# Kernel optimization log

Hardware: AMD Instinct MI355X
Metric: run time of the kernel (lower is better)

The kernel has to match this reference:

```python
import jax, jax.numpy as jnp
import numpy as np

N = 21  # nodes per graph (20 laser sectors + 1 robot node)
MAX_RANGE = 10.0
_bound = np.linspace(-np.pi / 2 - 0.03, np.pi / 2, 21, dtype=np.float32)[:-1]
_angles = _bound + np.float32(np.pi / 20)
ANGLE_FEAT = jnp.asarray(np.stack([np.sin(_angles), np.cos(_angles)], 1), dtype=jnp.float32)  # [20,2]


def _build_nodes(state24):
    # state24: [B,24] -> node features [B,21,7]
    B = state24.shape[0]
    laser = state24[:, :20, None] / MAX_RANGE                       # [B,20,1]
    angle = jnp.broadcast_to(ANGLE_FEAT[None], (B, 20, 2))          # [B,20,2]
    sector = jnp.concatenate([laser, angle, jnp.zeros((B, 20, 4), state24.dtype)], -1)  # [B,20,7]
    robot = jnp.concatenate([jnp.zeros((B, 1, 3), state24.dtype), state24[:, None, 20:]], -1)  # [B,1,7]
    return jnp.concatenate([sector, robot], axis=1)                 # [B,21,7]


def _gatv2(x, Wl, Wr, att, bias, heads, dim):
    # GATv2 over a fully-connected graph with self-loops (dense all-pairs).
    # e_ij = att . leaky_relu(Wl x_j + Wr x_i); alpha = softmax_j; out_i = sum_j alpha_ij (Wl x_j)
    B = x.shape[0]
    gl = (x @ Wl).reshape(B, N, heads, dim)  # source transform [B,j,H,D]
    gr = (x @ Wr).reshape(B, N, heads, dim)  # target transform [B,i,H,D]
    s = jax.nn.leaky_relu(gl[:, None] + gr[:, :, None], negative_slope=0.2)  # [B,i,j,H,D]
    e = jnp.einsum('bijhd,hd->bijh', s, att)                                  # [B,i,j,H]
    alpha = jax.nn.softmax(e, axis=2)                                          # softmax over sources j
    out = jnp.einsum('bijh,bjhd->bihd', alpha, gl).reshape(B, N, heads * dim)
    return out + bias


def setup_inputs() -> dict:
    key = jax.random.key(0)
    ks = jax.random.split(key, 16)
    r = lambda k, shape, s: (jax.random.normal(k, shape, dtype=jnp.float32) * s)
    B = 1024
    return {
        'state24': jax.random.normal(ks[0], (B, 24), dtype=jnp.float32),
        'Wl1': r(ks[1], (7, 256), 0.3), 'Wr1': r(ks[2], (7, 256), 0.3),
        'att1': r(ks[3], (4, 64), 0.1), 'b1': r(ks[4], (256,), 0.02),
        'Wl2': r(ks[5], (256, 64), 0.06), 'Wr2': r(ks[6], (256, 64), 0.06),
        'att2': r(ks[7], (1, 64), 0.1), 'b2': r(ks[8], (64,), 0.02),
        'fc1_w': r(ks[9], (64, 256), 0.12), 'fc1_b': r(ks[10], (256,), 0.02),
        'fc2_w': r(ks[11], (256, 256), 0.06), 'fc2_b': r(ks[12], (256,), 0.02),
        'fc3_w': r(ks[13], (256, 2), 0.06), 'fc3_b': r(ks[14], (2,), 0.02),
    }


def reference(state24, Wl1, Wr1, att1, b1, Wl2, Wr2, att2, b2,
              fc1_w, fc1_b, fc2_w, fc2_b, fc3_w, fc3_b):
    x = _build_nodes(state24)                               # [B,21,7]
    h = jax.nn.elu(_gatv2(x, Wl1, Wr1, att1, b1, 4, 64))    # [B,21,256]
    h = _gatv2(h, Wl2, Wr2, att2, b2, 1, 64)                # [B,21,64]
    nfv = jnp.mean(h, axis=1)                               # global_mean_pool -> [B,64]
    h = jax.nn.relu(nfv @ fc1_w + fc1_b)
    h = jax.nn.relu(h @ fc2_w + fc2_b)
    return jnp.tanh(h @ fc3_w + fc3_b)                      # [B,2]
```

## Files before the change

kernel.cpp:

```cpp
#include <hip/hip_runtime.h>
#include <hip/hip_fp16.h>
#include <math.h>

#define PI_D 3.141592653589793

typedef _Float16 h2 __attribute__((ext_vector_type(2)));
typedef _Float16 h4 __attribute__((ext_vector_type(4)));
typedef unsigned short us4 __attribute__((ext_vector_type(4)));
typedef __fp16 f16v2 __attribute__((ext_vector_type(2)));

#define STR1 260
#define STR1H 130
#define STR1Q 65
#define STR2 66

static __device__ __forceinline__ h2 pack_h2(float a, float b) {
    return __builtin_bit_cast(h2, __builtin_amdgcn_cvt_pkrtz(a, b));
}

static __device__ __forceinline__ float fdot2(h2 a, h2 b, float c) {
    return __builtin_amdgcn_fdot2(__builtin_bit_cast(f16v2, a),
                                  __builtin_bit_cast(f16v2, b), c, false);
}

static __device__ __forceinline__ h4 habs4(h4 x) {
    us4 u = __builtin_bit_cast(us4, x);
    us4 m = {0x7fff, 0x7fff, 0x7fff, 0x7fff};
    return __builtin_bit_cast(h4, (us4)(u & m));
}

__global__ __launch_bounds__(256, 4) void actor_fused_kernel(
    const float* __restrict__ state24,
    const float* __restrict__ Wl1, const float* __restrict__ Wr1,
    const float* __restrict__ att1, const float* __restrict__ b1,
    const float* __restrict__ Wl2, const float* __restrict__ Wr2,
    const float* __restrict__ att2, const float* __restrict__ b2,
    const float* __restrict__ fc1_w, const float* __restrict__ fc1_b,
    const float* __restrict__ fc2_w, const float* __restrict__ fc2_b,
    const float* __restrict__ fc3_w, const float* __restrict__ fc3_b,
    float* __restrict__ out, int B)
{
    const int bix = blockIdx.x;
    if (bix >= B) return;
    const int tid = threadIdx.x;

    __shared__ float sinL[20], cosL[20], laserL[20], robotL[4];
    __shared__ __align__(16) h2 attLh[128];
    __shared__ __align__(16) float att2L[64];
    __shared__ __align__(16) _Float16 gr1h[24 * STR1];
    __shared__ __align__(16) union {
        struct { _Float16 gl1h[21 * STR1]; float eP[1764]; } p1;
        struct { float gl2[24 * STR2]; float gr2[24 * STR2]; float e2[24 * 21];
                 float part[4][64]; float nfv[64]; float ha[256]; float hb[256]; } p2;
    } U;

    if (tid < 20) {
        double step = (PI_D + 0.03) / 20.0;
        float bound = (float)(-PI_D / 2.0 - 0.03 + (double)tid * step);
        float ang = bound + (float)(PI_D / 20.0);
        sinL[tid] = sinf(ang);
        cosL[tid] = cosf(ang);
        laserL[tid] = state24[bix * 24 + tid] * 0.1f;
    }
    if (tid >= 32 && tid < 36) robotL[tid - 32] = state24[bix * 24 + 20 + (tid - 32)];
    if (tid < 128) {
        float2 ap = ((const float2*)att1)[tid];
        attLh[tid] = pack_h2(ap.x, ap.y);
    }
    if (tid < 64) att2L[tid] = att2[tid];
    __syncthreads();

    {
        float wl[7], wr[7];
        #pragma unroll
        for (int k = 0; k < 7; k++) { wl[k] = Wl1[k * 256 + tid]; wr[k] = Wr1[k * 256 + tid]; }
        #pragma unroll
        for (int n = 0; n < 20; n++) {
            float l = laserL[n], s = sinL[n], c = cosL[n];
            U.p1.gl1h[n * STR1 + tid] = (_Float16)(l * wl[0] + s * wl[1] + c * wl[2]);
            gr1h[n * STR1 + tid]     = (_Float16)(l * wr[0] + s * wr[1] + c * wr[2]);
        }
        float r0 = robotL[0], r1 = robotL[1], r2 = robotL[2], r3 = robotL[3];
        U.p1.gl1h[20 * STR1 + tid] = (_Float16)(r0 * wl[3] + r1 * wl[4] + r2 * wl[5] + r3 * wl[6]);
        gr1h[20 * STR1 + tid]     = (_Float16)(r0 * wr[3] + r1 * wr[4] + r2 * wr[5] + r3 * wr[6]);
    }
    __syncthreads();

    {
        const int h = tid >> 6;
        const int lane = tid & 63;
        h4 areg[16];
        const h4* attH4 = (const h4*)attLh + h * 16;
        #pragma unroll
        for (int q = 0; q < 16; ++q) areg[q] = attH4[q];

        for (int it = 0; it < 7; ++it) {
            int q = it * 64 + lane;
            if (q < 441) {
                int i = q / 21;
                int j = q - i * 21;
                const h4* gA4 = (const h4*)(U.p1.gl1h + j * STR1 + h * 64);
                const h4* gB4 = (const h4*)(gr1h + i * STR1 + h * 64);
                float l0 = 0.f, l1 = 0.f, m0 = 0.f, m1 = 0.f;
                #pragma unroll
                for (int dp = 0; dp < 16; ++dp) {
                    h4 x = gA4[dp] + gB4[dp];
                    h4 ax = habs4(x);
                    h2 xl = __builtin_shufflevector(x, x, 0, 1);
                    h2 xh = __builtin_shufflevector(x, x, 2, 3);
                    h2 al = __builtin_shufflevector(areg[dp], areg[dp], 0, 1);
                    h2 ah = __builtin_shufflevector(areg[dp], areg[dp], 2, 3);
                    h2 axl = __builtin_shufflevector(ax, ax, 0, 1);
                    h2 axh = __builtin_shufflevector(ax, ax, 2, 3);
                    l0 = fdot2(xl, al, l0); m0 = fdot2(axl, al, m0);
                    l1 = fdot2(xh, ah, l1); m1 = fdot2(axh, ah, m1);
                }
                U.p1.eP[h * 441 + q] = 0.6f * (l0 + l1) + 0.4f * (m0 + m1);
            }
        }
    }
    __syncthreads();

    if (tid < 84) {
        float* row = U.p1.eP + tid * 21;
        float m = row[0];
        #pragma unroll
        for (int j = 1; j < 21; j++) m = fmaxf(m, row[j]);
        float s = 0.f;
        #pragma unroll
        for (int j = 0; j < 21; j++) { float v = __expf(row[j] - m); row[j] = v; s += v; }
        float r = 1.f / s;
        #pragma unroll
        for (int j = 0; j < 21; j++) row[j] *= r;
    }
    __syncthreads();

    {
        h2 zz = {(_Float16)0.f, (_Float16)0.f};
        for (int z = tid; z < 384; z += 256)
            ((h2*)gr1h)[(21 + (z >> 7)) * STR1H + (z & 127)] = zz;

        int p = tid & 127, gi = tid >> 7;
        int h = p >> 5;
        float2 bb = ((const float2*)b1)[p];
        const h2* gcol = (const h2*)U.p1.gl1h + p;
        for (int i = gi; i < 21; i += 2) {
            const float* al = U.p1.eP + (h * 21 + i) * 21;
            float a0 = 0.f, a1 = 0.f;
            #pragma unroll
            for (int j = 0; j < 21; ++j) {
                float alpha = al[j];
                h2 gv = gcol[j * STR1H];
                a0 = fmaf(alpha, (float)gv.x, a0);
                a1 = fmaf(alpha, (float)gv.y, a1);
            }
            float v0 = a0 + bb.x, v1 = a1 + bb.y;
            v0 = v0 > 0.f ? v0 : __expf(v0) - 1.f;
            v1 = v1 > 0.f ? v1 : __expf(v1) - 1.f;
            h2 o; o.x = (_Float16)v0; o.y = (_Float16)v1;
            ((h2*)gr1h)[i * STR1H + p] = o;
        }
    }
    __syncthreads();

    {
        int c = tid & 63, g = tid >> 6;
        float accL[6] = {0, 0, 0, 0, 0, 0}, accR[6] = {0, 0, 0, 0, 0, 0};
        const h4* hrow4 = (const h4*)gr1h;
        const float* pwl = Wl2 + c;
        const float* pwr = Wr2 + c;
        #pragma unroll 2
        for (int kk = 0; kk < 64; ++kk) {
            float wl0 = pwl[(4 * kk + 0) * 64], wl1 = pwl[(4 * kk + 1) * 64];
            float wl2_ = pwl[(4 * kk + 2) * 64], wl3 = pwl[(4 * kk + 3) * 64];
            float wr0 = pwr[(4 * kk + 0) * 64], wr1 = pwr[(4 * kk + 1) * 64];
            float wr2_ = pwr[(4 * kk + 2) * 64], wr3 = pwr[(4 * kk + 3) * 64];
            h2 wlA = pack_h2(wl0, wl1), wlB = pack_h2(wl2_, wl3);
            h2 wrA = pack_h2(wr0, wr1), wrB = pack_h2(wr2_, wr3);
            #pragma unroll
            for (int m = 0; m < 6; ++m) {
                int n = g + 4 * m;
                h4 hv = hrow4[n * STR1Q + kk];
                h2 lo = __builtin_shufflevector(hv, hv, 0, 1);
                h2 hi = __builtin_shufflevector(hv, hv, 2, 3);
                accL[m] = fdot2(lo, wlA, accL[m]);
                accL[m] = fdot2(hi, wlB, accL[m]);
                accR[m] = fdot2(lo, wrA, accR[m]);
                accR[m] = fdot2(hi, wrB, accR[m]);
            }
        }
        #pragma unroll
        for (int m = 0; m < 6; ++m) {
            int n = g + 4 * m;
            U.p2.gl2[n * STR2 + c] = accL[m];
            U.p2.gr2[n * STR2 + c] = accR[m];
        }
    }
    __syncthreads();

    for (int it = 0; it < 2; ++it) {
        int t = it * 256 + tid;
        if (t < 441) {
            int i = t / 21;
            int j = t - i * 21;
            const float2* gA = (const float2*)(U.p2.gl2 + j * STR2);
            const float2* gB = (const float2*)(U.p2.gr2 + i * STR2);
            const float2* aa = (const float2*)att2L;
            float l0 = 0.f, l1 = 0.f, m0 = 0.f, m1 = 0.f;
            #pragma unroll
            for (int dp = 0; dp < 32; ++dp) {
                float2 va = gA[dp], vb = gB[dp], a = aa[dp];
                float x0 = va.x + vb.x, x1 = va.y + vb.y;
                l0 = fmaf(a.x, x0, l0); m0 = fmaf(a.x, fabsf(x0), m0);
                l1 = fmaf(a.y, x1, l1); m1 = fmaf(a.y, fabsf(x1), m1);
            }
            U.p2.e2[t] = 0.6f * (l0 + l1) + 0.4f * (m0 + m1);
        }
    }
    __syncthreads();

    if (tid < 24) {
        float* row = U.p2.e2 + tid * 21;
        if (tid < 21) {
            float m = row[0];
            #pragma unroll
            for (int j = 1; j < 21; j++) m = fmaxf(m, row[j]);
            float s = 0.f;
            #pragma unroll
            for (int j = 0; j < 21; j++) { float v = __expf(row[j] - m); row[j] = v; s += v; }
            float r = 1.f / s;
            #pragma unroll
            for (int j = 0; j < 21; j++) row[j] *= r;
        } else {
            #pragma unroll
            for (int j = 0; j < 21; j++) row[j] = 0.f;
        }
    }
    __syncthreads();

    {
        int d = tid & 63, g = tid >> 6;
        float sacc = 0.f;
        #pragma unroll
        for (int m = 0; m < 6; ++m) {
            int i = g + 4 * m;
            const float* al = U.p2.e2 + i * 21;
            float acc = 0.f;
            #pragma unroll
            for (int j = 0; j < 21; ++j) acc = fmaf(al[j], U.p2.gl2[j * STR2 + d], acc);
            sacc += acc;
        }
        U.p2.part[g][d] = sacc;
    }
    __syncthreads();
    if (tid < 64) {
        U.p2.nfv[tid] = (U.p2.part[0][tid] + U.p2.part[1][tid] + U.p2.part[2][tid] + U.p2.part[3][tid])
                        * (1.f / 21.f) + b2[tid];
    }
    __syncthreads();

    {
        float acc = fc1_b[tid];
        #pragma unroll
        for (int k = 0; k < 64; k++) acc = fmaf(U.p2.nfv[k], fc1_w[k * 256 + tid], acc);
        U.p2.ha[tid] = fmaxf(acc, 0.f);
    }
    __syncthreads();

    {
        float acc = fc2_b[tid];
        #pragma unroll 8
        for (int k = 0; k < 256; k++) acc = fmaf(U.p2.ha[k], fc2_w[k * 256 + tid], acc);
        U.p2.hb[tid] = fmaxf(acc, 0.f);
    }
    __syncthreads();

    if (tid < 128) {
        int o = tid >> 6, l = tid & 63;
        float s = 0.f;
        #pragma unroll
        for (int m = 0; m < 4; m++) { int k = l + 64 * m; s = fmaf(U.p2.hb[k], fc3_w[k * 2 + o], s); }
        #pragma unroll
        for (int off = 32; off >= 1; off >>= 1) s += __shfl_down(s, off, 64);
        if (l == 0) out[bix * 2 + o] = tanhf(s + fc3_b[o]);
    }
}

extern "C" void kernel_launch(void* const* d_in, const int* in_sizes, int n_in,
                              void* d_out, int out_size, void* d_ws, size_t ws_size,
                              hipStream_t stream) {
    const float* state24 = (const float*)d_in[0];
    const float* Wl1 = (const float*)d_in[1];
    const float* Wr1 = (const float*)d_in[2];
    const float* att1 = (const float*)d_in[3];
    const float* b1 = (const float*)d_in[4];
    const float* Wl2 = (const float*)d_in[5];
    const float* Wr2 = (const float*)d_in[6];
    const float* att2 = (const float*)d_in[7];
    const float* b2 = (const float*)d_in[8];
    const float* fc1_w = (const float*)d_in[9];
    const float* fc1_b = (const float*)d_in[10];
    const float* fc2_w = (const float*)d_in[11];
    const float* fc2_b = (const float*)d_in[12];
    const float* fc3_w = (const float*)d_in[13];
    const float* fc3_b = (const float*)d_in[14];
    float* out = (float*)d_out;

    int B = in_sizes[0] / 24;
    actor_fused_kernel<<<B, 256, 0, stream>>>(
        state24, Wl1, Wr1, att1, b1, Wl2, Wr2, att2, b2,
        fc1_w, fc1_b, fc2_w, fc2_b, fc3_w, fc3_b, out, B);
}
```

Baseline: 136.6 us.

## Split linear leaky-ReLU term into per-node dots, widen LDS loads, split-K FC layers

New measurement: 134.2 us. No clear change (-1.8%).

```diff
diff --git a/kernel.cpp b/kernel.cpp
--- a/kernel.cpp
+++ b/kernel.cpp
@@ -6,12 +6,13 @@
 
 typedef _Float16 h2 __attribute__((ext_vector_type(2)));
 typedef _Float16 h4 __attribute__((ext_vector_type(4)));
-typedef unsigned short us4 __attribute__((ext_vector_type(4)));
+typedef _Float16 h8 __attribute__((ext_vector_type(8)));
+typedef unsigned short us8 __attribute__((ext_vector_type(8)));
 typedef __fp16 f16v2 __attribute__((ext_vector_type(2)));
 
-#define STR1 260
-#define STR1H 130
-#define STR1Q 65
+#define STR1 264
+#define STR1H 132
+#define STR1O 33
 #define STR2 66
 
 static __device__ __forceinline__ h2 pack_h2(float a, float b) {
@@ -23,10 +24,10 @@
                                   __builtin_bit_cast(f16v2, b), c, false);
 }
 
-static __device__ __forceinline__ h4 habs4(h4 x) {
-    us4 u = __builtin_bit_cast(us4, x);
-    us4 m = {0x7fff, 0x7fff, 0x7fff, 0x7fff};
-    return __builtin_bit_cast(h4, (us4)(u & m));
+static __device__ __forceinline__ h8 habs8(h8 x) {
+    us8 u = __builtin_bit_cast(us8, x);
+    us8 m = {0x7fff, 0x7fff, 0x7fff, 0x7fff, 0x7fff, 0x7fff, 0x7fff, 0x7fff};
+    return __builtin_bit_cast(h8, (us8)(u & m));
 }
 
 __global__ __launch_bounds__(256, 4) void actor_fused_kernel(
@@ -49,9 +50,9 @@
     __shared__ __align__(16) float att2L[64];
     __shared__ __align__(16) _Float16 gr1h[24 * STR1];
     __shared__ __align__(16) union {
-        struct { _Float16 gl1h[21 * STR1]; float eP[1764]; } p1;
-        struct { float gl2[24 * STR2]; float gr2[24 * STR2]; float e2[24 * 21];
-                 float part[4][64]; float nfv[64]; float ha[256]; float hb[256]; } p2;
+        struct { _Float16 gl1h[21 * STR1]; float eP[1764]; float uv[168]; } p1;
+        struct { float gl2[24 * STR2]; float gr2[24 * STR2]; float e2[504];
+                 float red[4][256]; float nfv[64]; float ha[256]; float hb[256]; } p2;
     } U;
 
     if (tid < 20) {
@@ -86,36 +87,52 @@
     }
     __syncthreads();
 
+    if (tid < 168) {
+        int r = tid < 84 ? tid : tid - 84;
+        int h = r / 21, idx = r - h * 21;
+        const _Float16* rowp = (tid < 84 ? U.p1.gl1h : gr1h) + idx * STR1 + h * 64;
+        const h8* row8 = (const h8*)rowp;
+        const h2* ar = attLh + h * 32;
+        float l0 = 0.f, l1 = 0.f;
+        #pragma unroll
+        for (int ch = 0; ch < 8; ++ch) {
+            h8 g = row8[ch];
+            l0 = fdot2(__builtin_shufflevector(g, g, 0, 1), ar[ch * 4 + 0], l0);
+            l1 = fdot2(__builtin_shufflevector(g, g, 2, 3), ar[ch * 4 + 1], l1);
+            l0 = fdot2(__builtin_shufflevector(g, g, 4, 5), ar[ch * 4 + 2], l0);
+            l1 = fdot2(__builtin_shufflevector(g, g, 6, 7), ar[ch * 4 + 3], l1);
+        }
+        U.p1.uv[tid] = l0 + l1;
+    }
+    __syncthreads();
+
     {
         const int h = tid >> 6;
         const int lane = tid & 63;
-        h4 areg[16];
-        const h4* attH4 = (const h4*)attLh + h * 16;
-        #pragma unroll
-        for (int q = 0; q < 16; ++q) areg[q] = attH4[q];
+        h2 ar[32];
+        #pragma unroll
+        for (int q = 0; q < 32; ++q) ar[q] = attLh[h * 32 + q];
+        const float* uvU = U.p1.uv + h * 21;
+        const float* uvV = U.p1.uv + 84 + h * 21;
 
         for (int it = 0; it < 7; ++it) {
             int q = it * 64 + lane;
             if (q < 441) {
                 int i = q / 21;
                 int j = q - i * 21;
-                const h4* gA4 = (const h4*)(U.p1.gl1h + j * STR1 + h * 64);
-                const h4* gB4 = (const h4*)(gr1h + i * STR1 + h * 64);
-                float l0 = 0.f, l1 = 0.f, m0 = 0.f, m1 = 0.f;
+                const h8* gA8 = (const h8*)(U.p1.gl1h + j * STR1 + h * 64);
+                const h8* gB8 = (const h8*)(gr1h + i * STR1 + h * 64);
+                float m0 = 0.f, m1 = 0.f;
                 #pragma unroll
-                for (int dp = 0; dp < 16; ++dp) {
-                    h4 x = gA4[dp] + gB4[dp];
-                    h4 ax = habs4(x);
-                    h2 xl = __builtin_shufflevector(x, x, 0, 1);
-                    h2 xh = __builtin_shufflevector(x, x, 2, 3);
-                    h2 al = __builtin_shufflevector(areg[dp], areg[dp], 0, 1);
-                    h2 ah = __builtin_shufflevector(areg[dp], areg[dp], 2, 3);
-                    h2 axl = __builtin_shufflevector(ax, ax, 0, 1);
-                    h2 axh = __builtin_shufflevector(ax, ax, 2, 3);
-                    l0 = fdot2(xl, al, l0); m0 = fdot2(axl, al, m0);
-                    l1 = fdot2(xh, ah, l1); m1 = fdot2(axh, ah, m1);
+                for (int ch = 0; ch < 8; ++ch) {
+                    h8 x = gA8[ch] + gB8[ch];
+                    h8 ax = habs8(x);
+                    m0 = fdot2(__builtin_shufflevector(ax, ax, 0, 1), ar[ch * 4 + 0], m0);
+                    m1 = fdot2(__builtin_shufflevector(ax, ax, 2, 3), ar[ch * 4 + 1], m1);
+                    m0 = fdot2(__builtin_shufflevector(ax, ax, 4, 5), ar[ch * 4 + 2], m0);
+                    m1 = fdot2(__builtin_shufflevector(ax, ax, 6, 7), ar[ch * 4 + 3], m1);
                 }
-                U.p1.eP[h * 441 + q] = 0.6f * (l0 + l1) + 0.4f * (m0 + m1);
+                U.p1.eP[h * 441 + q] = 0.6f * (uvU[j] + uvV[i]) + 0.4f * (m0 + m1);
             }
         }
     }
@@ -166,27 +183,36 @@
     {
         int c = tid & 63, g = tid >> 6;
         float accL[6] = {0, 0, 0, 0, 0, 0}, accR[6] = {0, 0, 0, 0, 0, 0};
-        const h4* hrow4 = (const h4*)gr1h;
+        const h8* hrow8 = (const h8*)gr1h;
         const float* pwl = Wl2 + c;
         const float* pwr = Wr2 + c;
-        #pragma unroll 2
-        for (int kk = 0; kk < 64; ++kk) {
-            float wl0 = pwl[(4 * kk + 0) * 64], wl1 = pwl[(4 * kk + 1) * 64];
-            float wl2_ = pwl[(4 * kk + 2) * 64], wl3 = pwl[(4 * kk + 3) * 64];
-            float wr0 = pwr[(4 * kk + 0) * 64], wr1 = pwr[(4 * kk + 1) * 64];
-            float wr2_ = pwr[(4 * kk + 2) * 64], wr3 = pwr[(4 * kk + 3) * 64];
-            h2 wlA = pack_h2(wl0, wl1), wlB = pack_h2(wl2_, wl3);
-            h2 wrA = pack_h2(wr0, wr1), wrB = pack_h2(wr2_, wr3);
+        for (int ch = 0; ch < 32; ++ch) {
+            float wlv[8], wrv[8];
+            #pragma unroll
+            for (int r = 0; r < 8; ++r) {
+                wlv[r] = pwl[(8 * ch + r) * 64];
+                wrv[r] = pwr[(8 * ch + r) * 64];
+            }
+            h2 wlA = pack_h2(wlv[0], wlv[1]), wlB = pack_h2(wlv[2], wlv[3]);
+            h2 wlC = pack_h2(wlv[4], wlv[5]), wlD = pack_h2(wlv[6], wlv[7]);
+            h2 wrA = pack_h2(wrv[0], wrv[1]), wrB = pack_h2(wrv[2], wrv[3]);
+            h2 wrC = pack_h2(wrv[4], wrv[5]), wrD = pack_h2(wrv[6], wrv[7]);
             #pragma unroll
             for (int m = 0; m < 6; ++m) {
                 int n = g + 4 * m;
-                h4 hv = hrow4[n * STR1Q + kk];
-                h2 lo = __builtin_shufflevector(hv, hv, 0, 1);
-                h2 hi = __builtin_shufflevector(hv, hv, 2, 3);
-                accL[m] = fdot2(lo, wlA, accL[m]);
-                accL[m] = fdot2(hi, wlB, accL[m]);
-                accR[m] = fdot2(lo, wrA, accR[m]);
-                accR[m] = fdot2(hi, wrB, accR[m]);
+                h8 hv = hrow8[n * STR1O + ch];
+                h2 s0 = __builtin_shufflevector(hv, hv, 0, 1);
+                h2 s1 = __builtin_shufflevector(hv, hv, 2, 3);
+                h2 s2 = __builtin_shufflevector(hv, hv, 4, 5);
+                h2 s3 = __builtin_shufflevector(hv, hv, 6, 7);
+                accL[m] = fdot2(s0, wlA, accL[m]);
+                accL[m] = fdot2(s1, wlB, accL[m]);
+                accL[m] = fdot2(s2, wlC, accL[m]);
+                accL[m] = fdot2(s3, wlD, accL[m]);
+                accR[m] = fdot2(s0, wrA, accR[m]);
+                accR[m] = fdot2(s1, wrB, accR[m]);
+                accR[m] = fdot2(s2, wrC, accR[m]);
+                accR[m] = fdot2(s3, wrD, accR[m]);
             }
         }
         #pragma unroll
@@ -250,28 +276,60 @@
             for (int j = 0; j < 21; ++j) acc = fmaf(al[j], U.p2.gl2[j * STR2 + d], acc);
             sacc += acc;
         }
-        U.p2.part[g][d] = sacc;
+        U.p2.red[g][d] = sacc;
     }
     __syncthreads();
     if (tid < 64) {
-        U.p2.nfv[tid] = (U.p2.part[0][tid] + U.p2.part[1][tid] + U.p2.part[2][tid] + U.p2.part[3][tid])
+        U.p2.nfv[tid] = (U.p2.red[0][tid] + U.p2.red[1][tid] + U.p2.red[2][tid] + U.p2.red[3][tid])
                         * (1.f / 21.f) + b2[tid];
     }
     __syncthreads();
 
     {
-        float acc = fc1_b[tid];
-        #pragma unroll
-        for (int k = 0; k < 64; k++) acc = fmaf(U.p2.nfv[k], fc1_w[k * 256 + tid], acc);
-        U.p2.ha[tid] = fmaxf(acc, 0.f);
-    }
-    __syncthreads();
-
-    {
-        float acc = fc2_b[tid];
+        int c = tid & 63, g = tid >> 6;
+        const float4* w4 = (const float4*)fc1_w;
+        float4 acc = {0.f, 0.f, 0.f, 0.f};
+        #pragma unroll
+        for (int kk = 0; kk < 16; ++kk) {
+            int k = g * 16 + kk;
+            float xv = U.p2.nfv[k];
+            float4 w = w4[k * 64 + c];
+            acc.x = fmaf(xv, w.x, acc.x);
+            acc.y = fmaf(xv, w.y, acc.y);
+            acc.z = fmaf(xv, w.z, acc.z);
+            acc.w = fmaf(xv, w.w, acc.w);
+        }
+        ((float4*)U.p2.red[g])[c] = acc;
+    }
+    __syncthreads();
+    {
+        float v = U.p2.red[0][tid] + U.p2.red[1][tid] + U.p2.red[2][tid] + U.p2.red[3][tid]
+                  + fc1_b[tid];
+        U.p2.ha[tid] = fmaxf(v, 0.f);
+    }
+    __syncthreads();
+
+    {
+        int c = tid & 63, g = tid >> 6;
+        const float4* w4 = (const float4*)fc2_w;
+        float4 acc = {0.f, 0.f, 0.f, 0.f};
         #pragma unroll 8
-        for (int k = 0; k < 256; k++) acc = fmaf(U.p2.ha[k], fc2_w[k * 256 + tid], acc);
-        U.p2.hb[tid] = fmaxf(acc, 0.f);
+        for (int kk = 0; kk < 64; ++kk) {
+            int k = g * 64 + kk;
+            float xv = U.p2.ha[k];
+            float4 w = w4[k * 64 + c];
+            acc.x = fmaf(xv, w.x, acc.x);
+            acc.y = fmaf(xv, w.y, acc.y);
+            acc.z = fmaf(xv, w.z, acc.z);
+            acc.w = fmaf(xv, w.w, acc.w);
+        }
+        ((float4*)U.p2.red[g])[c] = acc;
+    }
+    __syncthreads();
+    {
+        float v = U.p2.red[0][tid] + U.p2.red[1][tid] + U.p2.red[2][tid] + U.p2.red[3][tid]
+                  + fc2_b[tid];
+        U.p2.hb[tid] = fmaxf(v, 0.f);
     }
     __syncthreads();
 
```
